# Kernel tuning notes

Hardware: AMD Instinct MI355X
Metric: run time of the kernel (lower is better)

## Reference

```python
import jax, jax.numpy as jnp
import numpy as np

CORNER_MASK = jnp.array(
    [[0, 0, 0], [0, 0, 1], [0, 1, 0], [0, 1, 1],
     [1, 0, 0], [1, 0, 1], [1, 1, 0], [1, 1, 1]], dtype=jnp.float32)


def setup_inputs() -> dict:
    key = jax.random.key(0)
    k1, k2, k3, k4 = jax.random.split(key, 4)
    DEPTH = 6
    G = 2 ** DEPTH            # 64 voxels per axis at depth 6
    C = 32                    # feature channels
    H = G * G * G             # 262144 octree nodes at depth 6
    N = 1_000_000             # query points (depth-7 node centers)

    data = jax.random.normal(k1, (1, C, H, 1), dtype=jnp.float32)
    # points scaled into [0, 2^depth]; last column is the batch id (single octree -> 0)
    xyz = jax.random.uniform(k2, (N, 3), dtype=jnp.float32) * G
    ids = jnp.zeros((N, 1), dtype=jnp.float32)
    pts = jnp.concatenate([xyz, ids], axis=1)

    # dense voxel -> node-index lookup emulating ocnn.octree_search_key;
    idx_grid = jax.random.randint(k3, (G, G, G), 0, H, dtype=jnp.int32)
    empty = jax.random.uniform(k4, (G, G, G)) < 0.1
    lut = jnp.where(empty, jnp.int32(-1), idx_grid)

    return {"data": data, "pts": pts, "lut": lut, "depth": DEPTH}


def reference(data, pts, lut, depth):
    # data: (1, C, H, 1); pts: (N, 4); lut: (G, G, G) int32; depth: python int
    G = 2 ** depth
    xyzf = pts[:, :3] - 0.5                      # (N, 3)
    xyzi = jnp.floor(xyzf)
    frac = xyzf - xyzi                           # (N, 3) fractional offsets

    corners = xyzi[:, None, :] + CORNER_MASK[None, :, :]   # (N, 8, 3)
    ci = corners.astype(jnp.int32)
    in_bounds = jnp.all((ci >= 0) & (ci < G), axis=-1)     # (N, 8)
    ci_safe = jnp.clip(ci, 0, G - 1)
    idx = lut[ci_safe[..., 0], ci_safe[..., 1], ci_safe[..., 2]]  # (N, 8)
    valid = in_bounds & (idx > -1)

    # trilinear weights: |prod((1 - mask) - frac)|, matching the torch code
    w = jnp.abs(jnp.prod((1.0 - CORNER_MASK)[None, :, :] - frac[:, None, :], axis=-1))
    w = jnp.where(valid, w, 0.0)                 # (N, 8)
    idx_safe = jnp.where(valid, idx, 0)

    feat = data[0, :, :, 0].T                    # (H, C)
    gathered = feat[idx_safe]                    # (N, 8, C)
    out = jnp.einsum('nk,nkc->nc', w, gathered)  # weighted accumulate
    norm = jnp.sum(w, axis=1, keepdims=True)     # (N, 1)
    out = out / (norm + 1e-10)
    return out.T[None, :, :, None]               # (1, C, N, 1)
```

## Files before the change

### kernel.cpp

```cpp
#include <hip/hip_runtime.h>
#include <hip/hip_fp16.h>


#define NCH 32

typedef float nvec4 __attribute__((ext_vector_type(4)));

__global__ __launch_bounds__(256) void octri_transpose_h(
    const float* __restrict__ data, __half* __restrict__ featH, int H) {
  __shared__ float tile[32][33];
  const int h0 = blockIdx.x * 32;
  const int tx = threadIdx.x;
  const int ty = threadIdx.y;
#pragma unroll
  for (int i = 0; i < 4; ++i) {
    int c = ty + 8 * i;
    tile[c][tx] =
        __builtin_nontemporal_load(&data[(size_t)c * H + h0 + tx]);
  }
  __syncthreads();
#pragma unroll
  for (int i = 0; i < 4; ++i) {
    int hl = ty + 8 * i;
    featH[(size_t)(h0 + hl) * NCH + tx] = __float2half(tile[tx][hl]);
  }
}

__global__ __launch_bounds__(256) void octri_gather2(
    const __half* __restrict__ featH,
    const float* __restrict__ pts, const int* __restrict__ lut,
    const int* __restrict__ depth_p, float* __restrict__ out, int N) {
  __shared__ int meta[256][17];

  const int pblk = blockIdx.x * 256;
  const int G = 1 << depth_p[0];

  {
    const int p = threadIdx.x;
    const int n = min(pblk + p, N - 1);
    const nvec4 pt =
        __builtin_nontemporal_load((const nvec4*)(pts + (size_t)n * 4));
    const float fx = pt.x - 0.5f, fy = pt.y - 0.5f, fz = pt.z - 0.5f;
    const float flx = floorf(fx), fly = floorf(fy), flz = floorf(fz);
    const int ix = (int)flx, iy = (int)fly, iz = (int)flz;
    const float rx = fx - flx, ry = fy - fly, rz = fz - flz;
    const float wx[2] = {1.f - rx, rx};
    const float wy[2] = {1.f - ry, ry};
    const float wz[2] = {1.f - rz, rz};
    const bool vx[2] = {(unsigned)ix < (unsigned)G,
                        (unsigned)(ix + 1) < (unsigned)G};
    const bool vy[2] = {(unsigned)iy < (unsigned)G,
                        (unsigned)(iy + 1) < (unsigned)G};
    const bool vz[2] = {(unsigned)iz < (unsigned)G,
                        (unsigned)(iz + 1) < (unsigned)G};

    int idx[8];
    float w[8], wsum = 0.f;
#pragma unroll
    for (int k = 0; k < 8; ++k) {
      const int bx = (k >> 2) & 1, by = (k >> 1) & 1, bz = k & 1;
      const bool inb = vx[bx] & vy[by] & vz[bz];
      int id = -1;
      if (inb)
        id = lut[((size_t)(ix + bx) * G + (iy + by)) * G + (iz + bz)];
      const bool valid = inb && (id > -1);
      float wk = wx[bx] * wy[by] * wz[bz];
      wk = valid ? wk : 0.f;
      idx[k] = valid ? id : 0;
      w[k] = wk;
      wsum += wk;
    }
    const float s = (pblk + p < N) ? (1.f / (wsum + 1e-10f)) : 0.f;
#pragma unroll
    for (int k = 0; k < 8; ++k) {
      meta[p][k] = idx[k];
      meta[p][8 + k] = __float_as_int(w[k] * s);
    }
  }
  __syncthreads();

  const int lane = threadIdx.x & 63;
  const int wid = threadIdx.x >> 6;
  const int j = lane & 3;
#pragma unroll
  for (int g = 0; g < 4; ++g) {
    const int p = (wid << 6) + (g << 4) + (lane >> 2);
    const int n = pblk + p;

    float acc[8] = {};
#pragma unroll
    for (int k = 0; k < 8; ++k) {
      const int id = meta[p][k];
      const float ws = __int_as_float(meta[p][8 + k]);
      const nvec4 hv = *(const nvec4*)(featH + (size_t)id * NCH + j * 8);
      const __half2* h2 = (const __half2*)&hv;
#pragma unroll
      for (int q = 0; q < 4; ++q) {
        const float2 f = __half22float2(h2[q]);
        acc[2 * q + 0] += ws * f.x;
        acc[2 * q + 1] += ws * f.y;
      }
    }
    if (n < N) {
#pragma unroll
      for (int q = 0; q < 8; ++q) {
        __builtin_nontemporal_store(acc[q],
                                    &out[(size_t)(8 * j + q) * N + n]);
      }
    }
  }
}

__global__ __launch_bounds__(256) void octri_gather_direct(
    const float* __restrict__ data, const float* __restrict__ pts,
    const int* __restrict__ lut, const int* __restrict__ depth_p,
    float* __restrict__ out, int N, int H) {
  const int n = blockIdx.x * blockDim.x + threadIdx.x;
  if (n >= N) return;
  const int G = 1 << depth_p[0];

  const float4 p = ((const float4*)pts)[n];
  const float fx = p.x - 0.5f, fy = p.y - 0.5f, fz = p.z - 0.5f;
  const float flx = floorf(fx), fly = floorf(fy), flz = floorf(fz);
  const int ix = (int)flx, iy = (int)fly, iz = (int)flz;
  const float rx = fx - flx, ry = fy - fly, rz = fz - flz;
  const float wx[2] = {1.f - rx, rx};
  const float wy[2] = {1.f - ry, ry};
  const float wz[2] = {1.f - rz, rz};

  int idx[8];
  float w[8], wsum = 0.f;
#pragma unroll
  for (int k = 0; k < 8; ++k) {
    const int bx = (k >> 2) & 1, by = (k >> 1) & 1, bz = k & 1;
    const int cx = ix + bx, cy = iy + by, cz = iz + bz;
    const bool inb = (cx >= 0) & (cx < G) & (cy >= 0) & (cy < G) &
                     (cz >= 0) & (cz < G);
    int id = -1;
    if (inb) id = lut[((size_t)cx * G + cy) * G + cz];
    const bool valid = inb && (id > -1);
    float wk = wx[bx] * wy[by] * wz[bz];
    wk = valid ? wk : 0.f;
    idx[k] = valid ? id : 0;
    w[k] = wk;
    wsum += wk;
  }

  const float s = 1.f / (wsum + 1e-10f);
#pragma unroll 4
  for (int c = 0; c < NCH; ++c) {
    const float* plane = data + (size_t)c * H;
    float a = 0.f;
#pragma unroll
    for (int k = 0; k < 8; ++k) a += w[k] * plane[idx[k]];
    out[(size_t)c * N + n] = a * s;
  }
}

extern "C" void kernel_launch(void* const* d_in, const int* in_sizes, int n_in,
                              void* d_out, int out_size, void* d_ws,
                              size_t ws_size, hipStream_t stream) {
  const float* data = (const float*)d_in[0];
  const float* pts = (const float*)d_in[1];
  const int* lut = (const int*)d_in[2];
  const int* depth_p = (const int*)d_in[3];
  float* out = (float*)d_out;

  const int H = in_sizes[0] / NCH;
  const int N = in_sizes[1] / 4;

  const size_t need = (size_t)H * NCH * sizeof(__half);

  if (ws_size >= need) {
    __half* featH = (__half*)d_ws;
    dim3 tb(32, 8);
    octri_transpose_h<<<H / 32, tb, 0, stream>>>(data, featH, H);
    const int blocks = (N + 255) / 256;
    octri_gather2<<<blocks, 256, 0, stream>>>(featH, pts, lut, depth_p, out,
                                              N);
  } else {
    octri_gather_direct<<<(N + 255) / 256, 256, 0, stream>>>(
        data, pts, lut, depth_p, out, N, H);
  }
}
```

Baseline: 274.3 us.

## Pre-voxelize features into dense grid order with occupancy bitmask before gathering

Adds a voxelize kernel that copies each voxel's half-precision feature row into a dense grid-ordered buffer, using the output buffer as scratch for the transposed features. It also builds a 64-bit occupancy mask per (x,y) row. The gather kernel then reads the mask instead of doing eight random lut lookups per point, and fetches corner features from spatially coherent addresses, so neighbouring points share cache lines. The cost is an extra full pass over the grid and a larger workspace, and the fast path only runs for G==64.

```diff
diff --git a/kernel.cpp b/kernel.cpp
--- a/kernel.cpp
+++ b/kernel.cpp
@@ -26,14 +26,47 @@
   }
 }
 
-__global__ __launch_bounds__(256) void octri_gather2(
-    const __half* __restrict__ featH,
-    const float* __restrict__ pts, const int* __restrict__ lut,
-    const int* __restrict__ depth_p, float* __restrict__ out, int N) {
+__global__ __launch_bounds__(256) void octri_voxelize(
+    const __half* __restrict__ featH, const int* __restrict__ lut,
+    __half* __restrict__ featV, unsigned long long* __restrict__ vmask) {
+  const int t = threadIdx.x;
+  const int zi = t >> 2;
+  const int j = t & 3;
+  const int v = blockIdx.x * 64 + zi;
+  const int id = lut[v];
+
+  nvec4 row = {0.f, 0.f, 0.f, 0.f};
+  if (id >= 0)
+    row = *(const nvec4*)(featH + ((size_t)id << 5) + (j << 3));
+  *(nvec4*)(featV + ((size_t)v << 5) + (j << 3)) = row;
+
+  const unsigned long long b = __ballot(id >= 0);
+  unsigned int comp = 0;
+#pragma unroll
+  for (int k = 0; k < 16; ++k)
+    comp |= ((unsigned)(b >> (4 * k)) & 1u) << k;
+  __shared__ unsigned short sm16[4];
+  if ((t & 63) == 0) sm16[t >> 6] = (unsigned short)comp;
+  __syncthreads();
+  if (t == 0) {
+    unsigned long long m = (unsigned long long)sm16[0] |
+                           ((unsigned long long)sm16[1] << 16) |
+                           ((unsigned long long)sm16[2] << 32) |
+                           ((unsigned long long)sm16[3] << 48);
+    vmask[blockIdx.x] = m;
+  }
+}
+
+__global__ __launch_bounds__(256) void octri_gather3(
+    const __half* __restrict__ featV,
+    const unsigned long long* __restrict__ vmask,
+    const float* __restrict__ pts, const int* __restrict__ depth_p,
+    float* __restrict__ out, int N) {
   __shared__ int meta[256][17];
 
   const int pblk = blockIdx.x * 256;
   const int G = 1 << depth_p[0];
+  const int G1 = G - 1;
 
   {
     const int p = threadIdx.x;
@@ -53,6 +86,102 @@
                         (unsigned)(iy + 1) < (unsigned)G};
     const bool vz[2] = {(unsigned)iz < (unsigned)G,
                         (unsigned)(iz + 1) < (unsigned)G};
+    const int cxc[2] = {min(max(ix, 0), G1), min(max(ix + 1, 0), G1)};
+    const int cyc[2] = {min(max(iy, 0), G1), min(max(iy + 1, 0), G1)};
+    const int czc[2] = {min(max(iz, 0), G1), min(max(iz + 1, 0), G1)};
+
+    unsigned long long mrow[2][2];
+#pragma unroll
+    for (int bx = 0; bx < 2; ++bx)
+#pragma unroll
+      for (int by = 0; by < 2; ++by)
+        mrow[bx][by] = vmask[cxc[bx] * G + cyc[by]];
+
+    int vv[8];
+    float w[8], wsum = 0.f;
+#pragma unroll
+    for (int k = 0; k < 8; ++k) {
+      const int bx = (k >> 2) & 1, by = (k >> 1) & 1, bz = k & 1;
+      const bool valid = vx[bx] && vy[by] && vz[bz] &&
+                         (((mrow[bx][by] >> czc[bz]) & 1ull) != 0);
+      vv[k] = (cxc[bx] * G + cyc[by]) * G + czc[bz];
+      float wk = wx[bx] * wy[by] * wz[bz];
+      wk = valid ? wk : 0.f;
+      w[k] = wk;
+      wsum += wk;
+    }
+    const float s = (pblk + p < N) ? (1.f / (wsum + 1e-10f)) : 0.f;
+#pragma unroll
+    for (int k = 0; k < 8; ++k) {
+      meta[p][k] = vv[k];
+      meta[p][8 + k] = __float_as_int(w[k] * s);
+    }
+  }
+  __syncthreads();
+
+  const int lane = threadIdx.x & 63;
+  const int wid = threadIdx.x >> 6;
+  const int j = lane & 3;
+#pragma unroll
+  for (int g = 0; g < 4; ++g) {
+    const int p = (wid << 6) + (g << 4) + (lane >> 2);
+    const int n = pblk + p;
+
+    nvec4 r[8];
+    float ws[8];
+#pragma unroll
+    for (int k = 0; k < 8; ++k) {
+      const int v = meta[p][k];
+      ws[k] = __int_as_float(meta[p][8 + k]);
+      r[k] = *(const nvec4*)(featV + ((size_t)v << 5) + (j << 3));
+    }
+    float acc[8] = {};
+#pragma unroll
+    for (int k = 0; k < 8; ++k) {
+      const __half2* h2 = (const __half2*)&r[k];
+#pragma unroll
+      for (int q = 0; q < 4; ++q) {
+        const float2 f = __half22float2(h2[q]);
+        acc[2 * q + 0] += ws[k] * f.x;
+        acc[2 * q + 1] += ws[k] * f.y;
+      }
+    }
+    if (n < N) {
+#pragma unroll
+      for (int q = 0; q < 8; ++q) {
+        __builtin_nontemporal_store(acc[q],
+                                    &out[(size_t)(8 * j + q) * N + n]);
+      }
+    }
+  }
+}
+
+__global__ __launch_bounds__(256) void octri_gather2(
+    const __half* __restrict__ featH,
+    const float* __restrict__ pts, const int* __restrict__ lut,
+    const int* __restrict__ depth_p, float* __restrict__ out, int N) {
+  __shared__ int meta[256][17];
+  const int pblk = blockIdx.x * 256;
+  const int G = 1 << depth_p[0];
+
+  {
+    const int p = threadIdx.x;
+    const int n = min(pblk + p, N - 1);
+    const nvec4 pt =
+        __builtin_nontemporal_load((const nvec4*)(pts + (size_t)n * 4));
+    const float fx = pt.x - 0.5f, fy = pt.y - 0.5f, fz = pt.z - 0.5f;
+    const float flx = floorf(fx), fly = floorf(fy), flz = floorf(fz);
+    const int ix = (int)flx, iy = (int)fly, iz = (int)flz;
+    const float rx = fx - flx, ry = fy - fly, rz = fz - flz;
+    const float wx[2] = {1.f - rx, rx};
+    const float wy[2] = {1.f - ry, ry};
+    const float wz[2] = {1.f - rz, rz};
+    const bool vx[2] = {(unsigned)ix < (unsigned)G,
+                        (unsigned)(ix + 1) < (unsigned)G};
+    const bool vy[2] = {(unsigned)iy < (unsigned)G,
+                        (unsigned)(iy + 1) < (unsigned)G};
+    const bool vz[2] = {(unsigned)iz < (unsigned)G,
+                        (unsigned)(iz + 1) < (unsigned)G};
 
     int idx[8];
     float w[8], wsum = 0.f;
@@ -168,10 +297,29 @@
 
   const int H = in_sizes[0] / NCH;
   const int N = in_sizes[1] / 4;
-
-  const size_t need = (size_t)H * NCH * sizeof(__half);
-
-  if (ws_size >= need) {
+  const int SV = in_sizes[2];
+
+  int G = 1;
+  while ((size_t)(G + 1) * (G + 1) * (G + 1) <= (size_t)SV) ++G;
+
+  const size_t featH_bytes = (size_t)H * NCH * sizeof(__half);
+  const size_t featV_bytes = (size_t)SV * NCH * sizeof(__half);
+  const size_t needV = featV_bytes + (size_t)G * G * sizeof(unsigned long long);
+
+  if (G == 64 && (size_t)G * G * G == (size_t)SV && (H % 32) == 0 &&
+      ws_size >= needV &&
+      featH_bytes <= (size_t)out_size * sizeof(float)) {
+    __half* featH = (__half*)d_out;
+    __half* featV = (__half*)d_ws;
+    unsigned long long* vmask =
+        (unsigned long long*)((char*)d_ws + featV_bytes);
+    dim3 tb(32, 8);
+    octri_transpose_h<<<H / 32, tb, 0, stream>>>(data, featH, H);
+    octri_voxelize<<<SV / 64, 256, 0, stream>>>(featH, lut, featV, vmask);
+    const int blocks = (N + 255) / 256;
+    octri_gather3<<<blocks, 256, 0, stream>>>(featV, vmask, pts, depth_p,
+                                              out, N);
+  } else if (ws_size >= featH_bytes && (H % 32) == 0) {
     __half* featH = (__half*)d_ws;
     dim3 tb(32, 8);
     octri_transpose_h<<<H / 32, tb, 0, stream>>>(data, featH, H);
```

Measured after the change: 261.6 us. 1.05x faster.

## Precompute voxel-ordered z-pair feature rows and occupancy bitmasks for trilinear gather

Applied to the files above, without the earlier changes.

Adds a pass that reorders half-precision features into voxel order, storing each voxel's features together with its z+1 neighbour's in one 128-byte row, and builds per-(x,y) 64-bit occupancy masks from the lookup table. The gather kernel then fetches four pair rows per point instead of eight scattered node rows, and it no longer reads the lookup table because validity comes from the bitmasks. The intent is better locality and fewer indirect loads per query. The cost is an extra kernel plus a duplicated feature buffer, and the fast path is restricted to a 64^3 grid.

```diff
diff --git a/kernel.cpp b/kernel.cpp
--- a/kernel.cpp
+++ b/kernel.cpp
@@ -15,8 +15,7 @@
 #pragma unroll
   for (int i = 0; i < 4; ++i) {
     int c = ty + 8 * i;
-    tile[c][tx] =
-        __builtin_nontemporal_load(&data[(size_t)c * H + h0 + tx]);
+    tile[c][tx] = __builtin_nontemporal_load(&data[(size_t)c * H + h0 + tx]);
   }
   __syncthreads();
 #pragma unroll
@@ -26,14 +25,55 @@
   }
 }
 
-__global__ __launch_bounds__(256) void octri_gather2(
-    const __half* __restrict__ featH,
-    const float* __restrict__ pts, const int* __restrict__ lut,
-    const int* __restrict__ depth_p, float* __restrict__ out, int N) {
+__global__ __launch_bounds__(256) void octri_voxpair(
+    const __half* __restrict__ featH, const int* __restrict__ lut,
+    __half* __restrict__ featP, unsigned long long* __restrict__ vmask) {
+  __shared__ __half col[65][NCH];
+  __shared__ unsigned short sm16[4];
+  const int t = threadIdx.x;
+  const int zi = t >> 2;
+  const int j = t & 3;
+  const int v = blockIdx.x * 64 + zi;
+  const int id = __builtin_nontemporal_load(&lut[v]);
+
+  nvec4 r = {0.f, 0.f, 0.f, 0.f};
+  if (id >= 0)
+    r = __builtin_nontemporal_load(
+        (const nvec4*)(featH + ((size_t)id << 5) + (j << 3)));
+  *(nvec4*)(&col[zi][j << 3]) = r;
+  if (t < 4) *(nvec4*)(&col[64][t << 3]) = nvec4{0.f, 0.f, 0.f, 0.f};
+  __syncthreads();
+
+  const size_t rb = ((size_t)v << 6);
+  *(nvec4*)(featP + rb + (j << 3)) = r;
+  *(nvec4*)(featP + rb + 32 + (j << 3)) = *(const nvec4*)(&col[zi + 1][j << 3]);
+
+  const unsigned long long b = __ballot(id >= 0);
+  unsigned int comp = 0;
+#pragma unroll
+  for (int k = 0; k < 16; ++k)
+    comp |= ((unsigned)(b >> (4 * k)) & 1u) << k;
+  if ((t & 63) == 0) sm16[t >> 6] = (unsigned short)comp;
+  __syncthreads();
+  if (t == 0) {
+    unsigned long long m = (unsigned long long)sm16[0] |
+                           ((unsigned long long)sm16[1] << 16) |
+                           ((unsigned long long)sm16[2] << 32) |
+                           ((unsigned long long)sm16[3] << 48);
+    vmask[blockIdx.x] = m;
+  }
+}
+
+__global__ __launch_bounds__(256) void octri_gather7(
+    const __half* __restrict__ featP,
+    const unsigned long long* __restrict__ vmask,
+    const float* __restrict__ pts, const int* __restrict__ depth_p,
+    float* __restrict__ out, int N) {
   __shared__ int meta[256][17];
 
   const int pblk = blockIdx.x * 256;
   const int G = 1 << depth_p[0];
+  const int G1 = G - 1;
 
   {
     const int p = threadIdx.x;
@@ -53,29 +93,39 @@
                         (unsigned)(iy + 1) < (unsigned)G};
     const bool vz[2] = {(unsigned)iz < (unsigned)G,
                         (unsigned)(iz + 1) < (unsigned)G};
-
-    int idx[8];
+    const int cxc[2] = {min(max(ix, 0), G1), min(max(ix + 1, 0), G1)};
+    const int cyc[2] = {min(max(iy, 0), G1), min(max(iy + 1, 0), G1)};
+    const int czc[2] = {min(max(iz, 0), G1), min(max(iz + 1, 0), G1)};
+    const int zbase = czc[0];
+    const int h1 = czc[1] - zbase;
+
+    unsigned long long mrow[2][2];
+#pragma unroll
+    for (int bx = 0; bx < 2; ++bx)
+#pragma unroll
+      for (int by = 0; by < 2; ++by)
+        mrow[bx][by] = vmask[cxc[bx] * G + cyc[by]];
+
     float w[8], wsum = 0.f;
 #pragma unroll
     for (int k = 0; k < 8; ++k) {
       const int bx = (k >> 2) & 1, by = (k >> 1) & 1, bz = k & 1;
-      const bool inb = vx[bx] & vy[by] & vz[bz];
-      int id = -1;
-      if (inb)
-        id = lut[((size_t)(ix + bx) * G + (iy + by)) * G + (iz + bz)];
-      const bool valid = inb && (id > -1);
+      const bool valid = vx[bx] && vy[by] && vz[bz] &&
+                         (((mrow[bx][by] >> czc[bz]) & 1ull) != 0);
       float wk = wx[bx] * wy[by] * wz[bz];
       wk = valid ? wk : 0.f;
-      idx[k] = valid ? id : 0;
       w[k] = wk;
       wsum += wk;
     }
     const float s = (pblk + p < N) ? (1.f / (wsum + 1e-10f)) : 0.f;
 #pragma unroll
-    for (int k = 0; k < 8; ++k) {
-      meta[p][k] = idx[k];
-      meta[p][8 + k] = __float_as_int(w[k] * s);
-    }
+    for (int k = 0; k < 8; ++k) meta[p][k] = __float_as_int(w[k] * s);
+#pragma unroll
+    for (int q = 0; q < 4; ++q) {
+      const int bx = q >> 1, by = q & 1;
+      meta[p][8 + q] = (cxc[bx] * G + cyc[by]) * G + zbase;
+    }
+    meta[p][12] = h1 << 5;
   }
   __syncthreads();
 
@@ -86,26 +136,37 @@
   for (int g = 0; g < 4; ++g) {
     const int p = (wid << 6) + (g << 4) + (lane >> 2);
     const int n = pblk + p;
-
+    const int h1off = meta[p][12];
+
+    nvec4 r0[4], r1[4];
+    float ws0[4], ws1[4];
+#pragma unroll
+    for (int q = 0; q < 4; ++q) {
+      const int prow = meta[p][8 + q];
+      const __half* base = featP + ((size_t)prow << 6);
+      ws0[q] = __int_as_float(meta[p][2 * q]);
+      ws1[q] = __int_as_float(meta[p][2 * q + 1]);
+      r0[q] = *(const nvec4*)(base + (j << 3));
+      r1[q] = *(const nvec4*)(base + h1off + (j << 3));
+    }
     float acc[8] = {};
 #pragma unroll
-    for (int k = 0; k < 8; ++k) {
-      const int id = meta[p][k];
-      const float ws = __int_as_float(meta[p][8 + k]);
-      const nvec4 hv = *(const nvec4*)(featH + (size_t)id * NCH + j * 8);
-      const __half2* h2 = (const __half2*)&hv;
-#pragma unroll
-      for (int q = 0; q < 4; ++q) {
-        const float2 f = __half22float2(h2[q]);
-        acc[2 * q + 0] += ws * f.x;
-        acc[2 * q + 1] += ws * f.y;
+    for (int q = 0; q < 4; ++q) {
+      const __half2* a2 = (const __half2*)&r0[q];
+      const __half2* b2 = (const __half2*)&r1[q];
+#pragma unroll
+      for (int u = 0; u < 4; ++u) {
+        const float2 fa = __half22float2(a2[u]);
+        const float2 fb = __half22float2(b2[u]);
+        acc[2 * u + 0] += ws0[q] * fa.x + ws1[q] * fb.x;
+        acc[2 * u + 1] += ws0[q] * fa.y + ws1[q] * fb.y;
       }
     }
     if (n < N) {
 #pragma unroll
-      for (int q = 0; q < 8; ++q) {
-        __builtin_nontemporal_store(acc[q],
-                                    &out[(size_t)(8 * j + q) * N + n]);
+      for (int u = 0; u < 8; ++u) {
+        __builtin_nontemporal_store(acc[u],
+                                    &out[(size_t)(8 * j + u) * N + n]);
       }
     }
   }
@@ -118,7 +179,6 @@
   const int n = blockIdx.x * blockDim.x + threadIdx.x;
   if (n >= N) return;
   const int G = 1 << depth_p[0];
-
   const float4 p = ((const float4*)pts)[n];
   const float fx = p.x - 0.5f, fy = p.y - 0.5f, fz = p.z - 0.5f;
   const float flx = floorf(fx), fly = floorf(fy), flz = floorf(fz);
@@ -127,15 +187,14 @@
   const float wx[2] = {1.f - rx, rx};
   const float wy[2] = {1.f - ry, ry};
   const float wz[2] = {1.f - rz, rz};
-
   int idx[8];
   float w[8], wsum = 0.f;
 #pragma unroll
   for (int k = 0; k < 8; ++k) {
     const int bx = (k >> 2) & 1, by = (k >> 1) & 1, bz = k & 1;
     const int cx = ix + bx, cy = iy + by, cz = iz + bz;
-    const bool inb = (cx >= 0) & (cx < G) & (cy >= 0) & (cy < G) &
-                     (cz >= 0) & (cz < G);
+    const bool inb = (cx >= 0) & (cx < G) & (cy >= 0) & (cy < G) & (cz >= 0) &
+                     (cz < G);
     int id = -1;
     if (inb) id = lut[((size_t)cx * G + cy) * G + cz];
     const bool valid = inb && (id > -1);
@@ -145,7 +204,6 @@
     w[k] = wk;
     wsum += wk;
   }
-
   const float s = 1.f / (wsum + 1e-10f);
 #pragma unroll 4
   for (int c = 0; c < NCH; ++c) {
@@ -168,16 +226,39 @@
 
   const int H = in_sizes[0] / NCH;
   const int N = in_sizes[1] / 4;
-
-  const size_t need = (size_t)H * NCH * sizeof(__half);
-
-  if (ws_size >= need) {
-    __half* featH = (__half*)d_ws;
+  const int SV = in_sizes[2];
+
+  int G = 1;
+  while ((size_t)(G + 1) * (G + 1) * (G + 1) <= (size_t)SV) ++G;
+
+  const size_t featH_bytes = (size_t)H * NCH * sizeof(__half);
+  const size_t featP_bytes = (size_t)SV * 2 * NCH * sizeof(__half);
+  const size_t vmask_bytes = (size_t)G * G * sizeof(unsigned long long);
+
+  size_t offw = 0;
+  auto alloc = [&](size_t bytes) {
+    offw = (offw + 255) & ~(size_t)255;
+    size_t o = offw;
+    offw += bytes;
+    return o;
+  };
+  const size_t o_featH = alloc(featH_bytes);
+  const size_t o_featP = alloc(featP_bytes);
+  const size_t o_vmask = alloc(vmask_bytes);
+  const size_t need = offw;
+
+  if (G == 64 && (size_t)G * G * G == (size_t)SV && (H % 32) == 0 &&
+      ws_size >= need) {
+    char* ws = (char*)d_ws;
+    __half* featH = (__half*)(ws + o_featH);
+    __half* featP = (__half*)(ws + o_featP);
+    unsigned long long* vmask = (unsigned long long*)(ws + o_vmask);
+
     dim3 tb(32, 8);
     octri_transpose_h<<<H / 32, tb, 0, stream>>>(data, featH, H);
-    const int blocks = (N + 255) / 256;
-    octri_gather2<<<blocks, 256, 0, stream>>>(featH, pts, lut, depth_p, out,
-                                              N);
+    octri_voxpair<<<SV / 64, 256, 0, stream>>>(featH, lut, featP, vmask);
+    octri_gather7<<<(N + 255) / 256, 256, 0, stream>>>(featP, vmask, pts,
+                                                       depth_p, out, N);
   } else {
     octri_gather_direct<<<(N + 255) / 256, 256, 0, stream>>>(
         data, pts, lut, depth_p, out, N, H);
```

New measurement: 254.0 us. 1.08x faster.
